# Kernel tuning notes

Measured on AMD Instinct MI355X. Metric: run time of the kernel, lower is better.

Reference implementation:

```python
import jax, jax.numpy as jnp
import numpy as np

N_ROWS = 4096   # output features (N)
M_COLS = 4096   # input features (M)
BATCH = 4096
NNZ_PER_ROW = 819


def setup_inputs() -> dict:
    rng = np.random.default_rng(0)
    # sample NNZ_PER_ROW distinct, sorted column indices per row (CSR structure)
    cols = np.argsort(rng.random((N_ROWS, M_COLS)), axis=1)[:, :NNZ_PER_ROW]
    cols = np.sort(cols, axis=1).reshape(-1).astype(np.int32)            # [nnz]
    row_ids = np.repeat(np.arange(N_ROWS, dtype=np.int32), NNZ_PER_ROW)  # [nnz], expanded indptr

    key = jax.random.key(0)
    k1, k2, k3 = jax.random.split(key, 3)
    inp = jax.random.normal(k1, (BATCH, M_COLS), dtype=jnp.float32)
    W_val = jax.random.normal(k2, (N_ROWS * NNZ_PER_ROW,), dtype=jnp.float32) * 0.02
    bias = jax.random.normal(k3, (N_ROWS,), dtype=jnp.float32)
    return {
        "input": inp,
        "W_val": W_val,
        "bias": bias,
        "row_ids": jnp.asarray(row_ids),
        "cols": jnp.asarray(cols),
        "N": N_ROWS,
    }


def reference(input, W_val, bias, row_ids, cols, N):
    # Faithful math of SparseLinearFunction: y = x @ W^T + bias where W is the
    # CSR matrix (W_val, row_ids, cols) of shape (N, M). Densify via scatter
    # (CSR has unique (row, col) pairs) then use a single GEMM.
    M = input.shape[-1]
    W = jnp.zeros((N, M), dtype=W_val.dtype).at[row_ids, cols].set(W_val)  # [N, M]
    return jnp.matmul(input, W.T) + bias  # [B, N]
```

## Files before the change

### kernel.cpp

```cpp
#include <hip/hip_runtime.h>
#include <hip/hip_bf16.h>
#include <stdint.h>


#define B_DIM 4096
#define M_DIM 4096
#define N_DIM 4096
#define NNZ_ROW 819

typedef __attribute__((ext_vector_type(8))) __bf16 bf16x8;
typedef __attribute__((ext_vector_type(4))) float f32x4;

__device__ __forceinline__ unsigned short f32_to_bf16(float f) {
    union { float f; unsigned int u; } v;
    v.f = f;
    unsigned int r = v.u + 0x7FFFu + ((v.u >> 16) & 1u);
    return (unsigned short)(r >> 16);
}

__device__ __forceinline__ void load_lds16(const void* g, void* l) {
    __builtin_amdgcn_global_load_lds(
        (const __attribute__((address_space(1))) void*)g,
        (__attribute__((address_space(3))) void*)l,
        16, 0, 0);
}

__global__ __launch_bounds__(256) void densify_w(
    const float* __restrict__ wval,
    const int* __restrict__ cols,
    unsigned short* __restrict__ wb) {
    __shared__ __attribute__((aligned(16))) unsigned short row_s[M_DIM];
    const int row = blockIdx.x;
    const int tid = threadIdx.x;
    uint4* rs4 = (uint4*)row_s;
    rs4[tid]       = make_uint4(0u, 0u, 0u, 0u);
    rs4[tid + 256] = make_uint4(0u, 0u, 0u, 0u);
    __syncthreads();
    const size_t base = (size_t)row * NNZ_ROW;
    for (int j = tid; j < NNZ_ROW; j += 256) {
        const int c = cols[base + j];
        row_s[c] = f32_to_bf16(wval[base + j]);
    }
    __syncthreads();
    uint4* dst = (uint4*)(wb + (size_t)row * M_DIM);
    dst[tid]       = rs4[tid];
    dst[tid + 256] = rs4[tid + 256];
}

__global__ __launch_bounds__(256) void cvt_x_bf16(
    const float4* __restrict__ x, uint4* __restrict__ y, int n8) {
    int i = blockIdx.x * 256 + threadIdx.x;
    if (i >= n8) return;
    const float4 a = x[2 * i];
    const float4 b = x[2 * i + 1];
    union { ushort ush[8]; uint4 u4; } o;
    o.ush[0] = f32_to_bf16(a.x); o.ush[1] = f32_to_bf16(a.y);
    o.ush[2] = f32_to_bf16(a.z); o.ush[3] = f32_to_bf16(a.w);
    o.ush[4] = f32_to_bf16(b.x); o.ush[5] = f32_to_bf16(b.y);
    o.ush[6] = f32_to_bf16(b.z); o.ush[7] = f32_to_bf16(b.w);
    y[i] = o.u4;
}

__device__ __forceinline__ void stage_half(
    const unsigned short* __restrict__ src,
    int grow0,
    int kt,
    unsigned short* dst,
    int w, int l) {
#pragma unroll
    for (int j = 0; j < 2; ++j) {
        const int seg = w * 2 + j;
        const int r   = seg * 8 + (l >> 3);
        const int cg  = (l >> 3) ^ (l & 7);
        load_lds16(src + (size_t)(grow0 + r) * M_DIM + kt + cg * 8,
                   dst + seg * 512);
    }
}

template <int MA, int NB, int SK, int WAITN>
__device__ __forceinline__ void phase_op(
    const unsigned short* As_c, const unsigned short* Bs_c,
    unsigned short* As_n, unsigned short* Bs_n,
    const unsigned short* __restrict__ Xb, const unsigned short* __restrict__ Wb,
    int bm0, int bn0, int kn, bool do_stage,
    int wr, int wc, int w, int l, f32x4 (&acc)[2][4][2][2]) {
    const int l15 = l & 15;
    const int lg  = l >> 4;
    const int lx  = l & 7;
    const int ck0 = (lg ^ lx) << 3;
    const int ck1 = ((4 + lg) ^ lx) << 3;

    const unsigned short* Ab = As_c + (MA * 128 + wr * 64 + l15) * 64;
    const unsigned short* Bb = Bs_c + (NB * 128 + wc * 32 + l15) * 64;

    bf16x8 af[4][2], bfr[2][2];
#pragma unroll
    for (int mf = 0; mf < 4; ++mf) {
        af[mf][0] = *(const bf16x8*)(Ab + mf * 1024 + ck0);
        af[mf][1] = *(const bf16x8*)(Ab + mf * 1024 + ck1);
    }
#pragma unroll
    for (int nf = 0; nf < 2; ++nf) {
        bfr[nf][0] = *(const bf16x8*)(Bb + nf * 1024 + ck0);
        bfr[nf][1] = *(const bf16x8*)(Bb + nf * 1024 + ck1);
    }

    if (do_stage) {
        if constexpr (SK == 0) {
            stage_half(Xb, bm0,       kn, As_n,        w, l);
            stage_half(Wb, bn0,       kn, Bs_n,        w, l);
        }
        if constexpr (SK == 1) stage_half(Xb, bm0 + 128, kn, As_n + 8192, w, l);
        if constexpr (SK == 2) stage_half(Wb, bn0 + 128, kn, Bs_n + 8192, w, l);
    }

    if constexpr (WAITN >= 0) __builtin_amdgcn_s_waitcnt(0x0F70 | WAITN);
    __builtin_amdgcn_s_barrier();

    __builtin_amdgcn_s_setprio(1);
#pragma unroll
    for (int mf = 0; mf < 4; ++mf)
#pragma unroll
        for (int nf = 0; nf < 2; ++nf) {
            acc[MA][mf][NB][nf] = __builtin_amdgcn_mfma_f32_16x16x32_bf16(
                af[mf][0], bfr[nf][0], acc[MA][mf][NB][nf], 0, 0, 0);
            acc[MA][mf][NB][nf] = __builtin_amdgcn_mfma_f32_16x16x32_bf16(
                af[mf][1], bfr[nf][1], acc[MA][mf][NB][nf], 0, 0, 0);
        }
    __builtin_amdgcn_s_setprio(0);
    __builtin_amdgcn_s_barrier();
    __builtin_amdgcn_sched_barrier(0);
}

__global__ __launch_bounds__(512, 2) void gemm_bt_bias(
    const unsigned short* __restrict__ Xb,
    const unsigned short* __restrict__ Wb,
    const float* __restrict__ bias,
    float* __restrict__ out)
{
    __shared__ __attribute__((aligned(16))) unsigned short As0[16384];
    __shared__ __attribute__((aligned(16))) unsigned short Bs0[16384];
    __shared__ __attribute__((aligned(16))) unsigned short As1[16384];
    __shared__ __attribute__((aligned(16))) unsigned short Bs1[16384];

    const int tid = threadIdx.x;
    const int w   = tid >> 6;
    const int l   = tid & 63;
    const int wr  = w >> 2;
    const int wc  = w & 3;

    const int wg  = blockIdx.y * 16 + blockIdx.x;
    const int idx = ((wg & 7) << 5) | (wg >> 3);
    const int bm0 = (idx >> 4) * 256;
    const int bn0 = (idx & 15) * 256;

    f32x4 acc[2][4][2][2];
#pragma unroll
    for (int a = 0; a < 2; ++a)
#pragma unroll
        for (int b = 0; b < 4; ++b)
#pragma unroll
            for (int c = 0; c < 2; ++c)
#pragma unroll
                for (int d = 0; d < 2; ++d) acc[a][b][c][d] = (f32x4)0.0f;

    stage_half(Xb, bm0,       0, As0,        w, l);
    stage_half(Wb, bn0,       0, Bs0,        w, l);
    stage_half(Xb, bm0 + 128, 0, As0 + 8192, w, l);
    stage_half(Wb, bn0 + 128, 0, Bs0 + 8192, w, l);
    __builtin_amdgcn_s_waitcnt(0x0F70);
    __builtin_amdgcn_s_barrier();

#pragma unroll 1
    for (int kt = 0; kt < M_DIM; kt += 128) {
        const int k1 = kt + 64;
        const int k2 = kt + 128;
        const bool s2 = (k2 < M_DIM);
        phase_op<0,0,0, 6>(As0,Bs0, As1,Bs1, Xb,Wb, bm0,bn0, k1, true, wr,wc,w,l, acc);
        phase_op<1,0,1, 6>(As0,Bs0, As1,Bs1, Xb,Wb, bm0,bn0, k1, true, wr,wc,w,l, acc);
        phase_op<1,1,2,-1>(As0,Bs0, As1,Bs1, Xb,Wb, bm0,bn0, k1, true, wr,wc,w,l, acc);
        phase_op<0,1,3, 4>(As0,Bs0, As1,Bs1, Xb,Wb, bm0,bn0, k1, true, wr,wc,w,l, acc);
        phase_op<0,0,0, 6>(As1,Bs1, As0,Bs0, Xb,Wb, bm0,bn0, k2, s2,   wr,wc,w,l, acc);
        phase_op<1,0,1, 6>(As1,Bs1, As0,Bs0, Xb,Wb, bm0,bn0, k2, s2,   wr,wc,w,l, acc);
        phase_op<1,1,2,-1>(As1,Bs1, As0,Bs0, Xb,Wb, bm0,bn0, k2, s2,   wr,wc,w,l, acc);
        phase_op<0,1,3, 4>(As1,Bs1, As0,Bs0, Xb,Wb, bm0,bn0, k2, s2,   wr,wc,w,l, acc);
    }

    const int l15 = l & 15;
    const int lg  = l >> 4;
#pragma unroll
    for (int nb = 0; nb < 2; ++nb)
#pragma unroll
        for (int nf = 0; nf < 2; ++nf) {
            const int col = bn0 + nb * 128 + wc * 32 + nf * 16 + l15;
            const float bv = bias[col];
#pragma unroll
            for (int ma = 0; ma < 2; ++ma)
#pragma unroll
                for (int mf = 0; mf < 4; ++mf) {
                    const int row0 = bm0 + ma * 128 + wr * 64 + mf * 16 + lg * 4;
#pragma unroll
                    for (int r = 0; r < 4; ++r)
                        out[(size_t)(row0 + r) * N_DIM + col] =
                            acc[ma][mf][nb][nf][r] + bv;
                }
        }
}


extern "C" void kernel_launch(void* const* d_in, const int* in_sizes, int n_in,
                              void* d_out, int out_size, void* d_ws, size_t ws_size,
                              hipStream_t stream) {
    const float* x       = (const float*)d_in[0];
    const float* wval    = (const float*)d_in[1];
    const float* bias    = (const float*)d_in[2];
    const int*   cols    = (const int*)d_in[4];
    float* out = (float*)d_out;

    unsigned short* Wb = (unsigned short*)d_ws;
    unsigned short* Xb = Wb + (size_t)N_DIM * M_DIM;

    densify_w<<<dim3(N_DIM), dim3(256), 0, stream>>>(wval, cols, Wb);
    {
        int n8 = (B_DIM * M_DIM) / 8;
        cvt_x_bf16<<<dim3(n8 / 256), dim3(256), 0, stream>>>(
            (const float4*)x, (uint4*)Xb, n8);
    }
    gemm_bt_bias<<<dim3(N_DIM / 256, B_DIM / 256), dim3(512), 0, stream>>>(
        Xb, Wb, bias, out);
}
```

Measured before the change: 306.0 us.

## Fuse prep kernels and restructure GEMM phases to split K and reuse B fragments

Merges the W densify and X bf16 conversion into one launch to save a kernel launch and let the two overlap. The GEMM inner loop is reorganised so each phase handles one 32-wide K slice across both N halves, and the B fragments are read once per K slice and reused across both M halves, which cuts LDS reads. The staging order and waitcnt values are changed to match, and the final K tile is peeled so it skips staging. The cost is more register pressure from the persistent B fragments and tighter waitcnt ordering that must stay correct.

```diff
diff --git a/kernel.cpp b/kernel.cpp
--- a/kernel.cpp
+++ b/kernel.cpp
@@ -25,13 +25,27 @@
         16, 0, 0);
 }
 
-__global__ __launch_bounds__(256) void densify_w(
+__global__ __launch_bounds__(256) void prep(
     const float* __restrict__ wval,
     const int* __restrict__ cols,
-    unsigned short* __restrict__ wb) {
+    unsigned short* __restrict__ wb,
+    const float4* __restrict__ x,
+    uint4* __restrict__ xb) {
+    const int tid = threadIdx.x;
+    if (blockIdx.x >= N_DIM) {
+        const int i = (blockIdx.x - N_DIM) * 256 + tid;
+        const float4 a = x[2 * i];
+        const float4 b = x[2 * i + 1];
+        union { ushort ush[8]; uint4 u4; } o;
+        o.ush[0] = f32_to_bf16(a.x); o.ush[1] = f32_to_bf16(a.y);
+        o.ush[2] = f32_to_bf16(a.z); o.ush[3] = f32_to_bf16(a.w);
+        o.ush[4] = f32_to_bf16(b.x); o.ush[5] = f32_to_bf16(b.y);
+        o.ush[6] = f32_to_bf16(b.z); o.ush[7] = f32_to_bf16(b.w);
+        xb[i] = o.u4;
+        return;
+    }
     __shared__ __attribute__((aligned(16))) unsigned short row_s[M_DIM];
     const int row = blockIdx.x;
-    const int tid = threadIdx.x;
     uint4* rs4 = (uint4*)row_s;
     rs4[tid]       = make_uint4(0u, 0u, 0u, 0u);
     rs4[tid + 256] = make_uint4(0u, 0u, 0u, 0u);
@@ -47,26 +61,9 @@
     dst[tid + 256] = rs4[tid + 256];
 }
 
-__global__ __launch_bounds__(256) void cvt_x_bf16(
-    const float4* __restrict__ x, uint4* __restrict__ y, int n8) {
-    int i = blockIdx.x * 256 + threadIdx.x;
-    if (i >= n8) return;
-    const float4 a = x[2 * i];
-    const float4 b = x[2 * i + 1];
-    union { ushort ush[8]; uint4 u4; } o;
-    o.ush[0] = f32_to_bf16(a.x); o.ush[1] = f32_to_bf16(a.y);
-    o.ush[2] = f32_to_bf16(a.z); o.ush[3] = f32_to_bf16(a.w);
-    o.ush[4] = f32_to_bf16(b.x); o.ush[5] = f32_to_bf16(b.y);
-    o.ush[6] = f32_to_bf16(b.z); o.ush[7] = f32_to_bf16(b.w);
-    y[i] = o.u4;
-}
-
 __device__ __forceinline__ void stage_half(
     const unsigned short* __restrict__ src,
-    int grow0,
-    int kt,
-    unsigned short* dst,
-    int w, int l) {
+    int grow0, int kt, unsigned short* dst, int w, int l) {
 #pragma unroll
     for (int j = 0; j < 2; ++j) {
         const int seg = w * 2 + j;
@@ -77,32 +74,33 @@
     }
 }
 
-template <int MA, int NB, int SK, int WAITN>
+template <int MA, int KS, bool RDB, int SK, int WAITN>
 __device__ __forceinline__ void phase_op(
     const unsigned short* As_c, const unsigned short* Bs_c,
     unsigned short* As_n, unsigned short* Bs_n,
     const unsigned short* __restrict__ Xb, const unsigned short* __restrict__ Wb,
     int bm0, int bn0, int kn, bool do_stage,
-    int wr, int wc, int w, int l, f32x4 (&acc)[2][4][2][2]) {
+    int wr, int wc, int w, int l,
+    bf16x8 (&bfr)[2][2], f32x4 (&acc)[2][4][2][2]) {
     const int l15 = l & 15;
     const int lg  = l >> 4;
     const int lx  = l & 7;
-    const int ck0 = (lg ^ lx) << 3;
-    const int ck1 = ((4 + lg) ^ lx) << 3;
+    const int ck  = ((KS * 4 + lg) ^ lx) << 3;
 
     const unsigned short* Ab = As_c + (MA * 128 + wr * 64 + l15) * 64;
-    const unsigned short* Bb = Bs_c + (NB * 128 + wc * 32 + l15) * 64;
-
-    bf16x8 af[4][2], bfr[2][2];
-#pragma unroll
-    for (int mf = 0; mf < 4; ++mf) {
-        af[mf][0] = *(const bf16x8*)(Ab + mf * 1024 + ck0);
-        af[mf][1] = *(const bf16x8*)(Ab + mf * 1024 + ck1);
-    }
-#pragma unroll
-    for (int nf = 0; nf < 2; ++nf) {
-        bfr[nf][0] = *(const bf16x8*)(Bb + nf * 1024 + ck0);
-        bfr[nf][1] = *(const bf16x8*)(Bb + nf * 1024 + ck1);
+    bf16x8 af[4];
+#pragma unroll
+    for (int mf = 0; mf < 4; ++mf)
+        af[mf] = *(const bf16x8*)(Ab + mf * 1024 + ck);
+
+    if constexpr (RDB) {
+#pragma unroll
+        for (int nb = 0; nb < 2; ++nb) {
+            const unsigned short* Bb = Bs_c + (nb * 128 + wc * 32 + l15) * 64;
+#pragma unroll
+            for (int nf = 0; nf < 2; ++nf)
+                bfr[nb][nf] = *(const bf16x8*)(Bb + nf * 1024 + ck);
+        }
     }
 
     if (do_stage) {
@@ -110,8 +108,8 @@
             stage_half(Xb, bm0,       kn, As_n,        w, l);
             stage_half(Wb, bn0,       kn, Bs_n,        w, l);
         }
-        if constexpr (SK == 1) stage_half(Xb, bm0 + 128, kn, As_n + 8192, w, l);
-        if constexpr (SK == 2) stage_half(Wb, bn0 + 128, kn, Bs_n + 8192, w, l);
+        if constexpr (SK == 1) stage_half(Wb, bn0 + 128, kn, Bs_n + 8192, w, l);
+        if constexpr (SK == 2) stage_half(Xb, bm0 + 128, kn, As_n + 8192, w, l);
     }
 
     if constexpr (WAITN >= 0) __builtin_amdgcn_s_waitcnt(0x0F70 | WAITN);
@@ -121,12 +119,11 @@
 #pragma unroll
     for (int mf = 0; mf < 4; ++mf)
 #pragma unroll
-        for (int nf = 0; nf < 2; ++nf) {
-            acc[MA][mf][NB][nf] = __builtin_amdgcn_mfma_f32_16x16x32_bf16(
-                af[mf][0], bfr[nf][0], acc[MA][mf][NB][nf], 0, 0, 0);
-            acc[MA][mf][NB][nf] = __builtin_amdgcn_mfma_f32_16x16x32_bf16(
-                af[mf][1], bfr[nf][1], acc[MA][mf][NB][nf], 0, 0, 0);
-        }
+        for (int nb = 0; nb < 2; ++nb)
+#pragma unroll
+            for (int nf = 0; nf < 2; ++nf)
+                acc[MA][mf][nb][nf] = __builtin_amdgcn_mfma_f32_16x16x32_bf16(
+                    af[mf], bfr[nb][nf], acc[MA][mf][nb][nf], 0, 0, 0);
     __builtin_amdgcn_s_setprio(0);
     __builtin_amdgcn_s_barrier();
     __builtin_amdgcn_sched_barrier(0);
@@ -164,6 +161,8 @@
 #pragma unroll
                 for (int d = 0; d < 2; ++d) acc[a][b][c][d] = (f32x4)0.0f;
 
+    bf16x8 bfr[2][2];
+
     stage_half(Xb, bm0,       0, As0,        w, l);
     stage_half(Wb, bn0,       0, Bs0,        w, l);
     stage_half(Xb, bm0 + 128, 0, As0 + 8192, w, l);
@@ -171,20 +170,33 @@
     __builtin_amdgcn_s_waitcnt(0x0F70);
     __builtin_amdgcn_s_barrier();
 
+#define TILE4(AC, BC, AN, BN, KN, DS)                                          \
+    phase_op<0, 0, true , 0,  4>(AC, BC, AN, BN, Xb, Wb, bm0, bn0, KN, DS,     \
+                                 wr, wc, w, l, bfr, acc);                      \
+    phase_op<1, 0, false, 1, -1>(AC, BC, AN, BN, Xb, Wb, bm0, bn0, KN, DS,     \
+                                 wr, wc, w, l, bfr, acc);                      \
+    phase_op<0, 1, true , 2, -1>(AC, BC, AN, BN, Xb, Wb, bm0, bn0, KN, DS,     \
+                                 wr, wc, w, l, bfr, acc);                      \
+    phase_op<1, 1, false, 3,  2>(AC, BC, AN, BN, Xb, Wb, bm0, bn0, KN, DS,     \
+                                 wr, wc, w, l, bfr, acc);
+
 #pragma unroll 1
-    for (int kt = 0; kt < M_DIM; kt += 128) {
+    for (int kt = 0; kt < M_DIM - 128; kt += 128) {
         const int k1 = kt + 64;
         const int k2 = kt + 128;
-        const bool s2 = (k2 < M_DIM);
-        phase_op<0,0,0, 6>(As0,Bs0, As1,Bs1, Xb,Wb, bm0,bn0, k1, true, wr,wc,w,l, acc);
-        phase_op<1,0,1, 6>(As0,Bs0, As1,Bs1, Xb,Wb, bm0,bn0, k1, true, wr,wc,w,l, acc);
-        phase_op<1,1,2,-1>(As0,Bs0, As1,Bs1, Xb,Wb, bm0,bn0, k1, true, wr,wc,w,l, acc);
-        phase_op<0,1,3, 4>(As0,Bs0, As1,Bs1, Xb,Wb, bm0,bn0, k1, true, wr,wc,w,l, acc);
-        phase_op<0,0,0, 6>(As1,Bs1, As0,Bs0, Xb,Wb, bm0,bn0, k2, s2,   wr,wc,w,l, acc);
-        phase_op<1,0,1, 6>(As1,Bs1, As0,Bs0, Xb,Wb, bm0,bn0, k2, s2,   wr,wc,w,l, acc);
-        phase_op<1,1,2,-1>(As1,Bs1, As0,Bs0, Xb,Wb, bm0,bn0, k2, s2,   wr,wc,w,l, acc);
-        phase_op<0,1,3, 4>(As1,Bs1, As0,Bs0, Xb,Wb, bm0,bn0, k2, s2,   wr,wc,w,l, acc);
-    }
+        TILE4(As0, Bs0, As1, Bs1, k1, true)
+        TILE4(As1, Bs1, As0, Bs0, k2, true)
+    }
+    TILE4(As0, Bs0, As1, Bs1, M_DIM - 64, true)
+    phase_op<0, 0, true , 3,  0>(As1, Bs1, As0, Bs0, Xb, Wb, bm0, bn0, 0, false,
+                                 wr, wc, w, l, bfr, acc);
+    phase_op<1, 0, false, 3, -1>(As1, Bs1, As0, Bs0, Xb, Wb, bm0, bn0, 0, false,
+                                 wr, wc, w, l, bfr, acc);
+    phase_op<0, 1, true , 3, -1>(As1, Bs1, As0, Bs0, Xb, Wb, bm0, bn0, 0, false,
+                                 wr, wc, w, l, bfr, acc);
+    phase_op<1, 1, false, 3, -1>(As1, Bs1, As0, Bs0, Xb, Wb, bm0, bn0, 0, false,
+                                 wr, wc, w, l, bfr, acc);
+#undef TILE4
 
     const int l15 = l & 15;
     const int lg  = l >> 4;
@@ -220,12 +232,8 @@
     unsigned short* Wb = (unsigned short*)d_ws;
     unsigned short* Xb = Wb + (size_t)N_DIM * M_DIM;
 
-    densify_w<<<dim3(N_DIM), dim3(256), 0, stream>>>(wval, cols, Wb);
-    {
-        int n8 = (B_DIM * M_DIM) / 8;
-        cvt_x_bf16<<<dim3(n8 / 256), dim3(256), 0, stream>>>(
-            (const float4*)x, (uint4*)Xb, n8);
-    }
+    prep<<<dim3(N_DIM + (B_DIM * M_DIM) / 8 / 256), dim3(256), 0, stream>>>(
+        wval, cols, Wb, (const float4*)x, (uint4*)Xb);
     gemm_bt_bias<<<dim3(N_DIM / 256, B_DIM / 256), dim3(512), 0, stream>>>(
         Xb, Wb, bias, out);
 }
```

After: 280.1 us. 1.09x faster.
